# Kernel optimization log

Hardware: AMD Instinct MI355X
Metric: run time of the kernel (lower is better)

## Reference

```python
import jax, jax.numpy as jnp
import numpy as np

B, S, DIM = 2, 2048, 2048
H = 16
Q_LORA, KV_LORA = 1536, 512
D_NOPE, D_ROPE, D_V = 128, 64, 128
D_QK = D_NOPE + D_ROPE  # 192
SCALE = D_QK ** -0.5
EPS = 1e-6
NEG = -1e30


def rmsnorm(x, w):
    return x * jax.lax.rsqrt(jnp.mean(x * x, axis=-1, keepdims=True) + EPS) * w


def apply_rope(x, cos, sin):
    # x: [..., S, ..., d] with adjacent-pair complex layout (torch view_as_complex)
    d2 = x.shape[-1] // 2
    xr = x.reshape(x.shape[:-1] + (d2, 2))
    x0, x1 = xr[..., 0], xr[..., 1]
    bshape = (1, cos.shape[0]) + (1,) * (x.ndim - 3) + (d2,)
    c, s = cos.reshape(bshape), sin.reshape(bshape)
    o0 = x0 * c - x1 * s
    o1 = x0 * s + x1 * c
    return jnp.stack([o0, o1], axis=-1).reshape(x.shape)


def setup_inputs() -> dict:
    key = jax.random.key(0)
    ks = jax.random.split(key, 6)
    inv_freq = 1.0 / (10000.0 ** (np.arange(0, D_ROPE, 2, dtype=np.float32) / D_ROPE))
    ang = np.arange(S, dtype=np.float32)[:, None] * inv_freq[None, :]  # [S, 32]
    return {
        "x": jax.random.normal(ks[0], (B, S, DIM), jnp.float32),
        "wq_a": jax.random.normal(ks[1], (Q_LORA, DIM), jnp.float32) * (DIM ** -0.5),
        "q_norm_w": jnp.ones((Q_LORA,), jnp.float32),
        "wq_b": jax.random.normal(ks[2], (H * D_QK, Q_LORA), jnp.float32) * (Q_LORA ** -0.5),
        "wkv_a": jax.random.normal(ks[3], (KV_LORA + D_ROPE, DIM), jnp.float32) * (DIM ** -0.5),
        "kv_norm_w": jnp.ones((KV_LORA,), jnp.float32),
        "wkv_b": jax.random.normal(ks[4], (H * (D_NOPE + D_V), KV_LORA), jnp.float32) * (KV_LORA ** -0.5),
        "wo": jax.random.normal(ks[5], (DIM, H * D_V), jnp.float32) * ((H * D_V) ** -0.5),
        "cos": jnp.asarray(np.cos(ang)),
        "sin": jnp.asarray(np.sin(ang)),
    }


def reference(x, wq_a, q_norm_w, wq_b, wkv_a, kv_norm_w, wkv_b, wo, cos, sin):
    b, s, _ = x.shape
    # low-rank query projection: wq_b(q_norm(wq_a(x)))
    q = jnp.einsum('bsd,rd->bsr', x, wq_a)
    q = rmsnorm(q, q_norm_w)
    q = jnp.einsum('bsr,or->bso', q, wq_b).reshape(b, s, H, D_QK)
    q_nope, q_pe = q[..., :D_NOPE], q[..., D_NOPE:]
    q_pe = apply_rope(q_pe, cos, sin)  # [b,s,h,64]

    # joint kv latent + rope key
    kv = jnp.einsum('bsd,od->bso', x, wkv_a)
    kv_c, k_pe = kv[..., :KV_LORA], kv[..., KV_LORA:]
    k_pe = apply_rope(k_pe, cos, sin)          # [b,t,64]
    kv_c = rmsnorm(kv_c, kv_norm_w)            # [b,t,c] latent kv cache

    # absorbed wkv_b: [H, d_nope+d_v, c]
    wkv_b_r = wkv_b.reshape(H, D_NOPE + D_V, KV_LORA)
    w_nope, w_v = wkv_b_r[:, :D_NOPE, :], wkv_b_r[:, D_NOPE:, :]

    q_abs = jnp.einsum('bshd,hdc->bshc', q_nope, w_nope)  # absorb K up-proj into q
    scores = (jnp.einsum('bshc,btc->bsht', q_abs, kv_c) +
              jnp.einsum('bshr,btr->bsht', q_pe, k_pe)) * SCALE

    causal = jnp.tril(jnp.ones((s, s), bool))  # [s, t]
    scores = jnp.where(causal[:, None, :], scores, NEG)

    attn = jax.nn.softmax(scores.astype(jnp.float32), axis=-1).astype(x.dtype)
    o = jnp.einsum('bsht,btc->bshc', attn, kv_c)       # attend in latent space
    o = jnp.einsum('bshc,hdc->bshd', o, w_v)           # absorb V up-proj
    out = jnp.einsum('bsf,of->bso', o.reshape(b, s, H * D_V), wo)
    return out
```

## Files before the change

### kernel.cpp

```cpp
#include <hip/hip_runtime.h>
#include <hip/hip_bf16.h>
#include <stdint.h>

#define B_    2
#define S_    2048
#define DIM_  2048
#define H_    16
#define QL_   1536
#define KVL_  512
#define DN_   128
#define DR_   64
#define DV_   128
#define DQK_  192
#define NKV_  576
#define NKVP_ 640
#define BS_   (B_*S_)
#define SCALE_ 0.07216878364870322f

typedef __hip_bfloat16 bf16;
typedef float f32x4 __attribute__((ext_vector_type(4)));
typedef short bf16x8 __attribute__((ext_vector_type(8)));

#define BMT 128
#define BNT 128
#define BKT 64

__device__ __forceinline__ void gload_lds16(const void* g, void* l) {
#if __has_builtin(__builtin_amdgcn_global_load_lds)
  __builtin_amdgcn_global_load_lds(
      (const __attribute__((address_space(1))) void*)g,
      (__attribute__((address_space(3))) void*)l, 16, 0, 0);
#else
  *(uint4*)l = *(const uint4*)g;
#endif
}

template <int K, int LDA, int LDB, int LDC, int FLAGS>
__global__ __launch_bounds__(512, 4) void gemm_t(
    const bf16* __restrict__ A, long saz,
    const bf16* __restrict__ Bm, long sbz,
    void* __restrict__ Cv, long scz)
{
  int z = blockIdx.z;
  A  += (long)z * saz;
  Bm += (long)z * sbz;
  long coff = (long)z * scz;

  int gx = gridDim.x;
  int lin = blockIdx.y * gx + blockIdx.x;
  int nwg = gx * gridDim.y;
  int wg = (lin & 7) * (nwg >> 3) + (lin >> 3);
  int ry = wg / gx, col0 = (wg % gx) * BNT;

  const long bbase = (FLAGS & 32)
      ? (((long)(col0 >> 7) * 256 + 128) * (long)LDB)
      : ((long)col0 * (long)LDB);

  int tid = threadIdx.x, lane = tid & 63, wave = tid >> 6;
  int wm = (wave >> 2) * 64, wn = (wave & 3) * 32;
  int quad = lane >> 4, l16 = lane & 15;

  __shared__ __align__(16) bf16 Asm[BMT * BKT];
  __shared__ __align__(16) bf16 Bsm[BNT * BKT];

  const int npass = (FLAGS & 16) ? 2 : 1;
  const int nty = gridDim.y * ((FLAGS & 16) ? 2 : 1);

  for (int p = 0; p < npass; ++p) {
    int rt = (p == 0) ? ry : (nty - 1 - ry);
    int row0 = rt * BMT;

    if (FLAGS & 2) { if (col0 > row0 + (BMT - 1)) continue; }
    int kend = K;
    if (FLAGS & 4) { int lim = row0 + BMT; if (lim < kend) kend = lim; }

    f32x4 acc[4][2] = {};

    for (int k0 = 0; k0 < kend; k0 += BKT) {
      __syncthreads();
#pragma unroll
      for (int t = 0; t < 2; ++t) {
        int c = (wave * 2 + t) * 64 + lane;
        int m = c >> 3, jx = c & 7, j = jx ^ (m & 7);
        gload_lds16(A  + (long)((row0 + m) * LDA + k0 + j * 8), Asm + c * 8);
        gload_lds16(Bm + bbase + (long)m * LDB + k0 + j * 8, Bsm + c * 8);
      }
      __syncthreads();
#pragma unroll
      for (int kk = 0; kk < BKT; kk += 32) {
        int jl = (kk >> 3) + quad;
        bf16x8 af[4], bfv[2];
#pragma unroll
        for (int i = 0; i < 4; ++i) {
          int m = wm + i * 16 + l16;
          af[i]  = *(const bf16x8*)(Asm + m * 64 + ((jl ^ (m & 7)) * 8));
        }
#pragma unroll
        for (int jn = 0; jn < 2; ++jn) {
          int n = wn + jn * 16 + l16;
          bfv[jn] = *(const bf16x8*)(Bsm + n * 64 + ((jl ^ (n & 7)) * 8));
        }
#pragma unroll
        for (int i = 0; i < 4; ++i)
#pragma unroll
          for (int jn = 0; jn < 2; ++jn)
            acc[i][jn] = __builtin_amdgcn_mfma_f32_16x16x32_bf16(af[i], bfv[jn], acc[i][jn], 0, 0, 0);
      }
    }

    if (FLAGS & 1) {
      float* C = (float*)Cv + coff;
#pragma unroll
      for (int i = 0; i < 4; ++i)
#pragma unroll
        for (int jn = 0; jn < 2; ++jn)
#pragma unroll
          for (int r = 0; r < 4; ++r) {
            int rr = row0 + wm + i * 16 + quad * 4 + r;
            int cc = col0 + wn + jn * 16 + l16;
            C[(long)rr * LDC + cc] = acc[i][jn][r];
          }
    } else if (FLAGS & 8) {
      bf16* C = (bf16*)Cv + coff;
#pragma unroll
      for (int i = 0; i < 4; ++i)
#pragma unroll
        for (int jn = 0; jn < 2; ++jn)
#pragma unroll
          for (int r = 0; r < 4; ++r) {
            int rr = row0 + wm + i * 16 + quad * 4 + r;
            int cc = col0 + wn + jn * 16 + l16;
            C[(long)rr * LDC + cc] = __float2bfloat16(acc[i][jn][r] * SCALE_);
          }
    } else if (FLAGS & 64) {
      bf16* C = (bf16*)Cv + coff;
#pragma unroll
      for (int i = 0; i < 4; ++i)
#pragma unroll
        for (int jn = 0; jn < 2; ++jn) {
          int rr = row0 + wm + i * 16 + quad * 4;
          int cc = col0 + wn + jn * 16 + l16;
          __align__(8) bf16 t4[4];
#pragma unroll
          for (int r = 0; r < 4; ++r) t4[r] = __float2bfloat16(acc[i][jn][r]);
          *(short4*)(C + (long)cc * LDC + rr) = *(const short4*)t4;
        }
    } else {
      bf16* C = (bf16*)Cv + coff;
#pragma unroll
      for (int i = 0; i < 4; ++i)
#pragma unroll
        for (int jn = 0; jn < 2; ++jn)
#pragma unroll
          for (int r = 0; r < 4; ++r) {
            int rr = row0 + wm + i * 16 + quad * 4 + r;
            int cc = col0 + wn + jn * 16 + l16;
            C[(long)rr * LDC + cc] = __float2bfloat16(acc[i][jn][r]);
          }
    }
  }
}

template <int K, int LDA, int LDB, int LDC, int FLAGS>
static inline void G(hipStream_t st, const bf16* A, long saz, const bf16* Bp, long sbz,
                     void* C, long scz, int M, int N, int Z) {
  int gy = M / BMT;
  if (FLAGS & 16) gy >>= 1;
  dim3 g(N / BNT, gy, Z);
  gemm_t<K, LDA, LDB, LDC, FLAGS><<<g, 512, 0, st>>>(A, saz, Bp, sbz, C, scz);
}

__device__ __forceinline__ float wsum(float v) {
#pragma unroll
  for (int o = 32; o > 0; o >>= 1) v += __shfl_down(v, o, 64);
  return v;
}

#define CVT_N0  8388608L
#define CVT_N1 11534336L
#define CVT_N2 16252928L
#define CVT_N3 18350080L
#define CVT_N4 22544384L
#define CVT_N5 23855104L
__device__ __forceinline__ void cvt8(const float* __restrict__ s, bf16* __restrict__ d) {
  float4 a = ((const float4*)s)[0], b = ((const float4*)s)[1];
  __align__(16) bf16 t[8];
  t[0] = __float2bfloat16(a.x); t[1] = __float2bfloat16(a.y);
  t[2] = __float2bfloat16(a.z); t[3] = __float2bfloat16(a.w);
  t[4] = __float2bfloat16(b.x); t[5] = __float2bfloat16(b.y);
  t[6] = __float2bfloat16(b.z); t[7] = __float2bfloat16(b.w);
  *(uint4*)d = *(const uint4*)t;
}
__global__ __launch_bounds__(256) void cvt_all(
    const float* __restrict__ x, const float* __restrict__ wq_a,
    const float* __restrict__ wq_b, const float* __restrict__ wkv_b,
    const float* __restrict__ wo, const float* __restrict__ wkv_a,
    bf16* __restrict__ xb, bf16* __restrict__ wqab, bf16* __restrict__ wqbb,
    bf16* __restrict__ wkvbb, bf16* __restrict__ wob, bf16* __restrict__ wkvab)
{
  const long ngrp = CVT_N5 / 8;
  for (long v = (long)blockIdx.x * 256 + threadIdx.x; v < ngrp; v += (long)gridDim.x * 256) {
    long i = v * 8;
    if (i < CVT_N0) {
      cvt8(x + i, xb + i);
    } else if (i < CVT_N1) {
      long j = i - CVT_N0; cvt8(wq_a + j, wqab + j);
    } else if (i < CVT_N2) {
      long j = i - CVT_N1; cvt8(wq_b + j, wqbb + j);
    } else if (i < CVT_N3) {
      long j = i - CVT_N2; cvt8(wkv_b + j, wkvbb + j);
    } else if (i < CVT_N4) {
      long j = i - CVT_N3; cvt8(wo + j, wob + j);
    } else {
      long j = i - CVT_N4;
      if (j < (long)NKV_ * DIM_) cvt8(wkv_a + j, wkvab + j);
      else { __align__(16) bf16 t[8] = {}; *(uint4*)(wkvab + j) = *(const uint4*)t; }
    }
  }
}

__global__ __launch_bounds__(256) void rmsnorm_qa(bf16* __restrict__ qa, const float* __restrict__ w) {
  long row = blockIdx.x;
  bf16* pr = qa + row * QL_;
  int tid = threadIdx.x, lane = tid & 63, wave = tid >> 6;
  float v[6]; float ss = 0.f;
#pragma unroll
  for (int k = 0; k < 6; ++k) { int c = tid + k * 256; v[k] = __bfloat162float(pr[c]); ss += v[k] * v[k]; }
  ss = wsum(ss);
  __shared__ float sred[4];
  if (lane == 0) sred[wave] = ss;
  __syncthreads();
  float tot = sred[0] + sred[1] + sred[2] + sred[3];
  float scl = rsqrtf(tot / (float)QL_ + 1e-6f);
#pragma unroll
  for (int k = 0; k < 6; ++k) { int c = tid + k * 256; pr[c] = __float2bfloat16(v[k] * scl * w[c]); }
}

__global__ __launch_bounds__(256) void kv_post(const float* __restrict__ kvraw, const float* __restrict__ kvw,
                                               const float* __restrict__ cosb, const float* __restrict__ sinb,
                                               bf16* __restrict__ kfull) {
  int bs = blockIdx.x;
  int s = bs & (S_ - 1);
  const float* rowp = kvraw + (long)bs * NKVP_;
  bf16* outp = kfull + (long)bs * NKV_;
  int tid = threadIdx.x, lane = tid & 63, wave = tid >> 6;
  float v0 = rowp[tid], v1 = rowp[tid + 256];
  float ss = v0 * v0 + v1 * v1;
  ss = wsum(ss);
  __shared__ float sred[4];
  if (lane == 0) sred[wave] = ss;
  __syncthreads();
  float tot = sred[0] + sred[1] + sred[2] + sred[3];
  float scl = rsqrtf(tot / (float)KVL_ + 1e-6f);
  outp[tid]       = __float2bfloat16(v0 * scl * kvw[tid]);
  outp[tid + 256] = __float2bfloat16(v1 * scl * kvw[tid + 256]);
  if (tid < 32) {
    float x0 = rowp[KVL_ + 2 * tid], x1 = rowp[KVL_ + 2 * tid + 1];
    float c = cosb[s * 32 + tid], sn = sinb[s * 32 + tid];
    outp[KVL_ + 2 * tid]     = __float2bfloat16(x0 * c - x1 * sn);
    outp[KVL_ + 2 * tid + 1] = __float2bfloat16(x0 * sn + x1 * c);
  }
}

__global__ __launch_bounds__(256) void rope_q(bf16* __restrict__ qb,
                                              const float* __restrict__ cosb,
                                              const float* __restrict__ sinb) {
  int tx = threadIdx.x & 31, ty = threadIdx.x >> 5;
  long row = (long)blockIdx.x * 8 + ty;
  long bs = row >> 4; int h = (int)(row & 15); int s = (int)(bs & (S_ - 1));
  bf16* p = qb + bs * (H_ * DQK_) + h * DQK_ + DN_;
  float x0 = __bfloat162float(p[2 * tx]), x1 = __bfloat162float(p[2 * tx + 1]);
  float c = cosb[s * 32 + tx], sn = sinb[s * 32 + tx];
  p[2 * tx]     = __float2bfloat16(x0 * c - x1 * sn);
  p[2 * tx + 1] = __float2bfloat16(x0 * sn + x1 * c);
}

__global__ __launch_bounds__(256) void kpe_fill(const bf16* __restrict__ kfull, bf16* __restrict__ kvabs) {
  const long n = (long)B_ * H_ * S_ * 64;
  for (long i = (long)blockIdx.x * 256 + threadIdx.x; i < n; i += (long)gridDim.x * 256) {
    int d = (int)(i & 63);
    long t = (i >> 6) & (S_ - 1);
    int h = (int)((i >> 17) & 15);
    int b = (int)(i >> 21);
    kvabs[(((long)(b * H_ + h) * S_) + t) * DQK_ + DN_ + d] =
        kfull[((long)b * S_ + t) * NKV_ + KVL_ + d];
  }
}

__global__ __launch_bounds__(256) void softmax_causal(bf16* __restrict__ sc) {
  int wave = threadIdx.x >> 6, lane = threadIdx.x & 63;
  int r = blockIdx.x * 4 + wave, z = blockIdx.y;
  bf16* row = sc + ((long)z * S_ + r) * S_;
  int wlen = (r & ~127) + 128;
  int base0 = lane * 8;

  float v[4][8];
  float mx = -3.0e38f;
#pragma unroll
  for (int c = 0; c < 4; ++c) {
    int cb = c * 512;
    if (cb <= r) {
      int base = cb + base0;
      __align__(16) bf16 t8[8];
      *(bf16x8*)t8 = *(const bf16x8*)(row + base);
      if (cb + 511 <= r) {
#pragma unroll
        for (int j = 0; j < 8; ++j) {
          float f = __bfloat162float(t8[j]);
          v[c][j] = f; mx = fmaxf(mx, f);
        }
      } else {
#pragma unroll
        for (int j = 0; j < 8; ++j) {
          float f = (base + j <= r) ? __bfloat162float(t8[j]) : -3.0e38f;
          v[c][j] = f; mx = fmaxf(mx, f);
        }
      }
    }
  }
#pragma unroll
  for (int o = 32; o > 0; o >>= 1) mx = fmaxf(mx, __shfl_xor(mx, o, 64));

  float s = 0.f;
#pragma unroll
  for (int c = 0; c < 4; ++c) {
    if (c * 512 <= r) {
#pragma unroll
      for (int j = 0; j < 8; ++j) {
        float e = __expf(v[c][j] - mx);
        v[c][j] = e; s += e;
      }
    }
  }
#pragma unroll
  for (int o = 32; o > 0; o >>= 1) s += __shfl_xor(s, o, 64);
  float inv = 1.f / s;

#pragma unroll
  for (int c = 0; c < 4; ++c) {
    int base = c * 512 + base0;
    if (c * 512 <= r && base < wlen) {
      __align__(16) bf16 t8[8];
#pragma unroll
      for (int j = 0; j < 8; ++j) t8[j] = __float2bfloat16(v[c][j] * inv);
      *(bf16x8*)(row + base) = *(const bf16x8*)t8;
    }
  }
}

template <int HC>
static void attn_loop(hipStream_t stream, const bf16* qb, const bf16* kvabs,
                      const bf16* VabsT,
                      bf16* ovb, bf16* scores_c) {
  const int nch = B_ * (H_ / HC);
  for (int ch = 0; ch < nch; ++ch) {
    int b = ch / (H_ / HC), hq = ch % (H_ / HC), h0 = hq * HC;

    G<DQK_, H_ * DQK_, DQK_, S_, 8 | 2>(stream,
        qb + (long)b * S_ * (H_ * DQK_) + (long)h0 * DQK_, DQK_,
        kvabs + (long)(b * H_ + h0) * S_ * DQK_, (long)S_ * DQK_,
        scores_c, (long)S_ * S_, S_, S_, HC);
    softmax_causal<<<dim3(S_ / 4, HC), 256, 0, stream>>>(scores_c);
    G<S_, S_, S_, H_ * DV_, 4 | 16>(stream,
        scores_c, (long)S_ * S_,
        VabsT + (long)b * S_ * S_ + (long)h0 * DV_ * S_, (long)DV_ * S_,
        ovb + (long)b * S_ * (H_ * DV_) + (long)h0 * DV_, DV_, S_, DV_, HC);
  }
}

extern "C" void kernel_launch(void* const* d_in, const int* in_sizes, int n_in,
                              void* d_out, int out_size, void* d_ws, size_t ws_size,
                              hipStream_t stream) {
  const float* x     = (const float*)d_in[0];
  const float* wq_a  = (const float*)d_in[1];
  const float* qnw   = (const float*)d_in[2];
  const float* wq_b  = (const float*)d_in[3];
  const float* wkv_a = (const float*)d_in[4];
  const float* kvnw  = (const float*)d_in[5];
  const float* wkv_b = (const float*)d_in[6];
  const float* wo    = (const float*)d_in[7];
  const float* cosb  = (const float*)d_in[8];
  const float* sinb  = (const float*)d_in[9];
  float* out = (float*)d_out;
  (void)in_sizes; (void)n_in; (void)out_size;

  int hc;
  if      (ws_size >= 235405312UL) hc = 16;
  else if (ws_size >= 168296448UL) hc = 8;
  else                             hc = 4;

  char* base = (char*)d_ws;
  long off = 0;
  auto at = [&](long bytes) { char* r = base + off; off += bytes; return r; };

  bf16* qb    = (bf16*)at(25165824L);
  bf16* ovb   = (bf16*)at(16777216L);
  bf16* kfull = (bf16*)at(4718592L);
  bf16* wkvbb = (bf16*)at(4194304L);
  bf16* wob   = (bf16*)at(8388608L);
  bf16* kvabs = (bf16*)at(25165824L);
  bf16* VabsT = (bf16*)at(16777216L);
  char* ov = base + off;

  bf16*  xb    = (bf16*) (ov);
  bf16*  wqab  = (bf16*) (ov + 16777216L);
  bf16*  wqbb  = (bf16*) (ov + 23068672L);
  bf16*  qa    = (bf16*) (ov + 32505856L);
  float* kvraw = (float*)qa;

  bf16* scores_c = (bf16*)ov;

  bf16* wkvab = VabsT;

  cvt_all<<<4096, 256, 0, stream>>>(x, wq_a, wq_b, wkv_b, wo, wkv_a,
                                    xb, wqab, wqbb, wkvbb, wob, wkvab);

  G<DIM_, DIM_, DIM_, QL_, 0>(stream, xb, 0, wqab, 0, qa, 0, BS_, QL_, 1);
  rmsnorm_qa<<<BS_, 256, 0, stream>>>(qa, qnw);
  G<QL_, QL_, QL_, H_ * DQK_, 0>(stream, qa, 0, wqbb, 0, qb, 0, BS_, H_ * DQK_, 1);
  rope_q<<<BS_ * H_ / 8, 256, 0, stream>>>(qb, cosb, sinb);

  G<DIM_, DIM_, DIM_, NKVP_, 1>(stream, xb, 0, wkvab, 0, kvraw, 0, BS_, NKVP_, 1);
  kv_post<<<BS_, 256, 0, stream>>>(kvraw, kvnw, cosb, sinb, kfull);

  for (int b = 0; b < B_; ++b)
    G<KVL_, NKV_, KVL_, DQK_, 0>(stream,
        kfull + (long)b * S_ * NKV_, 0, wkvbb, (long)256 * KVL_,
        kvabs + (long)b * H_ * S_ * DQK_, (long)S_ * DQK_, S_, DN_, H_);
  kpe_fill<<<8192, 256, 0, stream>>>(kfull, kvabs);

  G<KVL_, NKV_, KVL_, S_, 32 | 64>(stream,
      kfull, (long)S_ * NKV_, wkvbb, 0,
      VabsT, (long)S_ * S_, S_, H_ * DV_, B_);

  if (hc == 16)
    attn_loop<16>(stream, qb, kvabs, VabsT, ovb, scores_c);
  else if (hc == 8)
    attn_loop<8>(stream, qb, kvabs, VabsT, ovb, scores_c);
  else
    attn_loop<4>(stream, qb, kvabs, VabsT, ovb, scores_c);

  G<H_ * DV_, H_ * DV_, H_ * DV_, DIM_, 1>(stream, ovb, 0, wob, 0, out, 0, BS_, DIM_, 1);
}
```

Baseline: 543.5 us.

## Merge q_a/kv_a projections and fuse K-absorb with V-absorb GEMMs

New measurement: 517.9 us. 4.7% less time.

```diff
diff --git a/kernel.cpp b/kernel.cpp
--- a/kernel.cpp
+++ b/kernel.cpp
@@ -39,7 +39,8 @@
 __global__ __launch_bounds__(512, 4) void gemm_t(
     const bf16* __restrict__ A, long saz,
     const bf16* __restrict__ Bm, long sbz,
-    void* __restrict__ Cv, long scz)
+    void* __restrict__ Cv, long scz,
+    void* __restrict__ Cv2)
 {
   int z = blockIdx.z;
   A  += (long)z * saz;
@@ -52,10 +53,6 @@
   int wg = (lin & 7) * (nwg >> 3) + (lin >> 3);
   int ry = wg / gx, col0 = (wg % gx) * BNT;
 
-  const long bbase = (FLAGS & 32)
-      ? (((long)(col0 >> 7) * 256 + 128) * (long)LDB)
-      : ((long)col0 * (long)LDB);
-
   int tid = threadIdx.x, lane = tid & 63, wave = tid >> 6;
   int wm = (wave >> 2) * 64, wn = (wave & 3) * 32;
   int quad = lane >> 4, l16 = lane & 15;
@@ -83,7 +80,7 @@
         int c = (wave * 2 + t) * 64 + lane;
         int m = c >> 3, jx = c & 7, j = jx ^ (m & 7);
         gload_lds16(A  + (long)((row0 + m) * LDA + k0 + j * 8), Asm + c * 8);
-        gload_lds16(Bm + bbase + (long)m * LDB + k0 + j * 8, Bsm + c * 8);
+        gload_lds16(Bm + (long)((col0 + m) * LDB + k0 + j * 8), Bsm + c * 8);
       }
       __syncthreads();
 #pragma unroll
@@ -108,7 +105,61 @@
       }
     }
 
-    if (FLAGS & 1) {
+    if (FLAGS & 128) {
+      if (col0 < QL_) {
+        bf16* C = (bf16*)Cv;
+#pragma unroll
+        for (int i = 0; i < 4; ++i)
+#pragma unroll
+          for (int jn = 0; jn < 2; ++jn)
+#pragma unroll
+            for (int r = 0; r < 4; ++r) {
+              int rr = row0 + wm + i * 16 + quad * 4 + r;
+              int cc = col0 + wn + jn * 16 + l16;
+              C[(long)rr * QL_ + cc] = __float2bfloat16(acc[i][jn][r]);
+            }
+      } else {
+        float* C2 = (float*)Cv2;
+#pragma unroll
+        for (int i = 0; i < 4; ++i)
+#pragma unroll
+          for (int jn = 0; jn < 2; ++jn)
+#pragma unroll
+            for (int r = 0; r < 4; ++r) {
+              int rr = row0 + wm + i * 16 + quad * 4 + r;
+              int cc = col0 + wn + jn * 16 + l16 - QL_;
+              C2[(long)rr * NKVP_ + cc] = acc[i][jn][r];
+            }
+      }
+    } else if (FLAGS & 256) {
+      int cb = col0 >> 7, h = cb >> 1;
+      if ((cb & 1) == 0) {
+        bf16* C = (bf16*)Cv + ((long)z * H_ + h) * (long)S_ * DQK_;
+#pragma unroll
+        for (int i = 0; i < 4; ++i)
+#pragma unroll
+          for (int jn = 0; jn < 2; ++jn)
+#pragma unroll
+            for (int r = 0; r < 4; ++r) {
+              int rr = row0 + wm + i * 16 + quad * 4 + r;
+              int cc = (wn + jn * 16 + l16) & 127;
+              C[(long)rr * DQK_ + cc] = __float2bfloat16(acc[i][jn][r]);
+            }
+      } else {
+        bf16* C = (bf16*)Cv2 + (long)z * S_ * S_;
+#pragma unroll
+        for (int i = 0; i < 4; ++i)
+#pragma unroll
+          for (int jn = 0; jn < 2; ++jn) {
+            int rr = row0 + wm + i * 16 + quad * 4;
+            int nv = h * 128 + ((wn + jn * 16 + l16) & 127);
+            __align__(8) bf16 t4[4];
+#pragma unroll
+            for (int r = 0; r < 4; ++r) t4[r] = __float2bfloat16(acc[i][jn][r]);
+            *(short4*)(C + (long)nv * S_ + rr) = *(const short4*)t4;
+          }
+      }
+    } else if (FLAGS & 1) {
       float* C = (float*)Cv + coff;
 #pragma unroll
       for (int i = 0; i < 4; ++i)
@@ -132,19 +183,6 @@
             int cc = col0 + wn + jn * 16 + l16;
             C[(long)rr * LDC + cc] = __float2bfloat16(acc[i][jn][r] * SCALE_);
           }
-    } else if (FLAGS & 64) {
-      bf16* C = (bf16*)Cv + coff;
-#pragma unroll
-      for (int i = 0; i < 4; ++i)
-#pragma unroll
-        for (int jn = 0; jn < 2; ++jn) {
-          int rr = row0 + wm + i * 16 + quad * 4;
-          int cc = col0 + wn + jn * 16 + l16;
-          __align__(8) bf16 t4[4];
-#pragma unroll
-          for (int r = 0; r < 4; ++r) t4[r] = __float2bfloat16(acc[i][jn][r]);
-          *(short4*)(C + (long)cc * LDC + rr) = *(const short4*)t4;
-        }
     } else {
       bf16* C = (bf16*)Cv + coff;
 #pragma unroll
@@ -163,11 +201,11 @@
 
 template <int K, int LDA, int LDB, int LDC, int FLAGS>
 static inline void G(hipStream_t st, const bf16* A, long saz, const bf16* Bp, long sbz,
-                     void* C, long scz, int M, int N, int Z) {
+                     void* C, long scz, int M, int N, int Z, void* C2 = nullptr) {
   int gy = M / BMT;
   if (FLAGS & 16) gy >>= 1;
   dim3 g(N / BNT, gy, Z);
-  gemm_t<K, LDA, LDB, LDC, FLAGS><<<g, 512, 0, st>>>(A, saz, Bp, sbz, C, scz);
+  gemm_t<K, LDA, LDB, LDC, FLAGS><<<g, 512, 0, st>>>(A, saz, Bp, sbz, C, scz, C2);
 }
 
 __device__ __forceinline__ float wsum(float v) {
@@ -404,34 +442,28 @@
 
   bf16*  xb    = (bf16*) (ov);
   bf16*  wqab  = (bf16*) (ov + 16777216L);
-  bf16*  wqbb  = (bf16*) (ov + 23068672L);
-  bf16*  qa    = (bf16*) (ov + 32505856L);
-  float* kvraw = (float*)qa;
+  bf16*  wkvab = (bf16*) (ov + 23068672L);
+  bf16*  wqbb  = (bf16*) (ov + 25690112L);
+  bf16*  qa    = (bf16*) (ov + 35127296L);
+  float* kvraw = (float*)(ov + 47710208L);
 
   bf16* scores_c = (bf16*)ov;
-
-  bf16* wkvab = VabsT;
 
   cvt_all<<<4096, 256, 0, stream>>>(x, wq_a, wq_b, wkv_b, wo, wkv_a,
                                     xb, wqab, wqbb, wkvbb, wob, wkvab);
 
-  G<DIM_, DIM_, DIM_, QL_, 0>(stream, xb, 0, wqab, 0, qa, 0, BS_, QL_, 1);
+  G<DIM_, DIM_, DIM_, QL_, 128>(stream, xb, 0, wqab, 0,
+                                qa, 0, BS_, QL_ + NKVP_, 1, kvraw);
   rmsnorm_qa<<<BS_, 256, 0, stream>>>(qa, qnw);
+  kv_post<<<BS_, 256, 0, stream>>>(kvraw, kvnw, cosb, sinb, kfull);
+
   G<QL_, QL_, QL_, H_ * DQK_, 0>(stream, qa, 0, wqbb, 0, qb, 0, BS_, H_ * DQK_, 1);
   rope_q<<<BS_ * H_ / 8, 256, 0, stream>>>(qb, cosb, sinb);
 
-  G<DIM_, DIM_, DIM_, NKVP_, 1>(stream, xb, 0, wkvab, 0, kvraw, 0, BS_, NKVP_, 1);
-  kv_post<<<BS_, 256, 0, stream>>>(kvraw, kvnw, cosb, sinb, kfull);
-
-  for (int b = 0; b < B_; ++b)
-    G<KVL_, NKV_, KVL_, DQK_, 0>(stream,
-        kfull + (long)b * S_ * NKV_, 0, wkvbb, (long)256 * KVL_,
-        kvabs + (long)b * H_ * S_ * DQK_, (long)S_ * DQK_, S_, DN_, H_);
+  G<KVL_, NKV_, KVL_, DQK_, 256>(stream,
+      kfull, (long)S_ * NKV_, wkvbb, 0,
+      kvabs, 0, S_, H_ * 256, B_, VabsT);
   kpe_fill<<<8192, 256, 0, stream>>>(kfull, kvabs);
-
-  G<KVL_, NKV_, KVL_, S_, 32 | 64>(stream,
-      kfull, (long)S_ * NKV_, wkvbb, 0,
-      VabsT, (long)S_ * S_, S_, H_ * DV_, B_);
 
   if (hc == 16)
     attn_loop<16>(stream, qb, kvabs, VabsT, ovb, scores_c);
```
